# Kernel optimization log

Hardware: AMD Instinct MI355X
Metric: run time of the kernel (lower is better)

## Reference

```python
import jax, jax.numpy as jnp
import numpy as np

# Representative Blocks2Matrix configuration: single coupled block key
# (l1=2, l2=2, lambda=2), one atom type with 8 radial channels.
N_SYS = 16        # number of systems
N_ATOMS = 64      # atoms per system
L1, L2, LAM = 2, 2, 2
NRAD = 8          # radial channels per (l, Z)
S = 32768         # number of atom-pair samples across all systems
M1, M2, MU = 2 * L1 + 1, 2 * L2 + 1, 2 * LAM + 1
NORB_ATOM = NRAD * M1            # orbitals per atom (radial-major, mu-minor; see make_orbital_map)
N = N_ATOMS * NORB_ATOM          # 2560 orbitals per system


def setup_inputs() -> dict:
    key = jax.random.key(0)
    k1, k2, k3, k4, k5 = jax.random.split(key, 5)
    values = jax.random.normal(k1, (S, MU, NRAD * NRAD), dtype=jnp.float32)
    cg = jax.random.normal(k2, (M1, M2, MU), dtype=jnp.float32)
    sys_idx = jax.random.randint(k3, (S,), 0, N_SYS)
    i_idx = jax.random.randint(k4, (S,), 0, N_ATOMS)
    j_idx = jax.random.randint(k5, (S,), 0, N_ATOMS)
    return {"values": values, "cg": cg, "sys_idx": sys_idx,
            "i_idx": i_idx, "j_idx": j_idx}


def reference(values, cg, sys_idx, i_idx, j_idx):
    # Decouple: uncoupled[s, m1, m2, n1, n2] = sum_mu cg[m1, m2, mu] * values[s, mu, n1, n2]
    vals = values.reshape(S, MU, NRAD, NRAD)
    # orbital ordering is radial-major, mu-minor -> index (n, m)
    blocks = jnp.einsum('abm,smpq->spaqb', cg, vals)  # [S, n1, m1, n2, m2]
    blocks = blocks.reshape(S, NORB_ATOM, NORB_ATOM)
    # Global orbital indices for each pair's block rows/cols
    ar = jnp.arange(NORB_ATOM)
    rows = i_idx[:, None] * NORB_ATOM + ar  # [S, 40]
    cols = j_idx[:, None] * NORB_ATOM + ar  # [S, 40]
    H = jnp.zeros((N_SYS, N, N), dtype=values.dtype)
    # Scatter block at (i, j) and its transpose at (j, i) (Hermitian build)
    H = H.at[sys_idx[:, None, None], rows[:, :, None], cols[:, None, :]].add(blocks)
    H = H.at[sys_idx[:, None, None], cols[:, :, None], rows[:, None, :]].add(
        jnp.swapaxes(blocks, 1, 2))
    return H
```

## Files before the change

kernel.cpp:

```cpp
#include <hip/hip_runtime.h>


#define SS      32768
#define NORB    40
#define NSYS    16
#define NATOMS  64
#define NDIM    2560
#define NBINS   (NSYS * NATOMS * NATOMS)
#define CAP     16
#define MAXOVF  8192
#define GBLK    2048
#define TPB     256
#define WPB     (TPB / 64)
#define BPW     (NBINS / (GBLK * WPB))

#define WS_NEEDED   (524288 + (size_t)NBINS * CAP * 4)

__global__ __launch_bounds__(256) void b2m_fill(
    const int* __restrict__ sys_idx, const int* __restrict__ i_idx,
    const int* __restrict__ j_idx,
    int* __restrict__ counts, int* __restrict__ bins,
    int* __restrict__ ovf_cnt, int2* __restrict__ ovf)
{
    int s = blockIdx.x * blockDim.x + threadIdx.x;
    if (s >= SS) return;
    int sy = sys_idx[s], i = i_idx[s], j = j_idx[s];

    int bd = (sy * NATOMS + i) * NATOMS + j;
    int pos = atomicAdd(&counts[bd], 1);
    if (pos < CAP) bins[bd * CAP + pos] = s;
    else { int o = atomicAdd(ovf_cnt, 1); if (o < MAXOVF) ovf[o] = make_int2(bd, s); }

    int bt = (sy * NATOMS + j) * NATOMS + i;
    int st = s | 0x10000;
    pos = atomicAdd(&counts[bt], 1);
    if (pos < CAP) bins[bt * CAP + pos] = st;
    else { int o = atomicAdd(ovf_cnt, 1); if (o < MAXOVF) ovf[o] = make_int2(bt, st); }
}

#define ENTRY_BODY(ENT) do {                                            \
    int _ent = (ENT);                                                   \
    const float* _vb = values + (size_t)(_ent & 0xFFFF) * 320;          \
    if ((_ent & 0x10000) == 0) {                                        \
        ++nD;                                                           \
        _Pragma("unroll")                                               \
        for (int m = 0; m < 5; ++m) vsD[m] += _vb[m * 64 + lane];       \
    } else {                                                            \
        ++nT;                                                           \
        _Pragma("unroll")                                               \
        for (int m = 0; m < 5; ++m) vsT[m] += _vb[m * 64 + bsl];        \
    }                                                                   \
} while (0)

__global__ __launch_bounds__(TPB) void b2m_gather(
    const float* __restrict__ values, const float* __restrict__ cg,
    const int* __restrict__ counts, const int* __restrict__ bins,
    float* __restrict__ H)
{
    __shared__ float scg[128];
    __shared__ float stage[WPB][320];

    const int tid  = threadIdx.x;
    const int lane = tid & 63;
    const int w    = tid >> 6;

    if (tid < 125) scg[tid] = cg[tid];
    __syncthreads();

    const int p   = lane >> 3, q = lane & 7;
    const int bsl = (q << 3) | p;

    int soff[5];
    #pragma unroll
    for (int it = 0; it < 5; ++it) {
        int e = it * 64 + lane;
        int srow = e / 40, scol = e - srow * 40;
        soff[it] = srow * 5 * NDIM + scol;
    }

    const int gw = __builtin_amdgcn_readfirstlane((int)blockIdx.x * WPB + w);
    const int t0 = gw * BPW;
    float* const sw = stage[w];

    for (int t = t0; t < t0 + BPW; ++t) {
        int n = counts[t];
        if (n > CAP) n = CAP;

        float vsD[5] = {0.f, 0.f, 0.f, 0.f, 0.f};
        float vsT[5] = {0.f, 0.f, 0.f, 0.f, 0.f};
        int nD = 0, nT = 0;

        if (n > 0) {
            int4 e4 = *reinterpret_cast<const int4*>(bins + (size_t)t * CAP);
            ENTRY_BODY(e4.x);
            if (n > 1) ENTRY_BODY(e4.y);
            if (n > 2) ENTRY_BODY(e4.z);
            if (n > 3) ENTRY_BODY(e4.w);
            for (int k = 4; k < n; ++k)
                ENTRY_BODY(bins[(size_t)t * CAP + k]);
        }

        float acc[25];
        #pragma unroll
        for (int i2 = 0; i2 < 25; ++i2) acc[i2] = 0.f;

        if (nD) {
            #pragma unroll
            for (int a = 0; a < 5; ++a)
                #pragma unroll
                for (int b = 0; b < 5; ++b)
                    #pragma unroll
                    for (int m = 0; m < 5; ++m)
                        acc[a * 5 + b] = fmaf(scg[(a * 5 + b) * 5 + m], vsD[m], acc[a * 5 + b]);
        }
        if (nT) {
            #pragma unroll
            for (int a = 0; a < 5; ++a)
                #pragma unroll
                for (int b = 0; b < 5; ++b)
                    #pragma unroll
                    for (int m = 0; m < 5; ++m)
                        acc[a * 5 + b] = fmaf(scg[(b * 5 + a) * 5 + m], vsT[m], acc[a * 5 + b]);
        }

        const int jj = t & 63, ii = (t >> 6) & 63, sy = t >> 12;
        float* Hs = H + ((size_t)sy * NDIM + (size_t)ii * NORB) * NDIM + (size_t)jj * NORB;
        #pragma unroll
        for (int g = 0; g < 5; ++g) {
            #pragma unroll
            for (int b = 0; b < 5; ++b)
                sw[p * 40 + q * 5 + b] = acc[g * 5 + b];
            #pragma unroll
            for (int it = 0; it < 5; ++it)
                Hs[(size_t)(soff[it] + g * NDIM)] = sw[it * 64 + lane];
        }
    }
}

__global__ __launch_bounds__(256) void b2m_ovf_apply(
    const float* __restrict__ values, const float* __restrict__ cg,
    const int* __restrict__ ovf_cnt, const int2* __restrict__ ovf,
    float* __restrict__ H)
{
    int n = *ovf_cnt;
    if (n > MAXOVF) n = MAXOVF;
    for (int k = blockIdx.x; k < n; k += gridDim.x) {
        int  bin = ovf[k].x;
        int  ent = ovf[k].y;
        int  s   = ent & 0xFFFF;
        bool tr  = (ent >> 16) != 0;
        int  j = bin & 63, i = (bin >> 6) & 63, sy = bin >> 12;
        const float* vs = values + (size_t)s * 320;
        float* Hs = H + (size_t)sy * NDIM * NDIM;
        for (int e = threadIdx.x; e < 1600; e += blockDim.x) {
            int rr = e / 40, cc = e - rr * 40;
            int R = tr ? cc : rr, C = tr ? rr : cc;
            int pp = R / 5, a = R - pp * 5;
            int qq = C / 5, b = C - qq * 5;
            float v = 0.f;
            for (int m = 0; m < 5; ++m)
                v = fmaf(cg[(a * 5 + b) * 5 + m], vs[m * 64 + pp * 8 + qq], v);
            atomicAdd(Hs + (size_t)(i * NORB + rr) * NDIM + (j * NORB + cc), v);
        }
    }
}

__global__ __launch_bounds__(320) void b2m_scatter(
    const float* __restrict__ values, const float* __restrict__ cg,
    const int* __restrict__ sys_idx, const int* __restrict__ i_idx,
    const int* __restrict__ j_idx, float* __restrict__ H)
{
    __shared__ float svv[320];
    __shared__ float scg[125];
    const int s = blockIdx.x, tid = threadIdx.x;
    if (tid < 320) svv[tid] = values[(size_t)s * 320 + tid];
    if (tid < 125) scg[tid] = cg[tid];
    __syncthreads();
    const int sys = sys_idx[s], i = i_idx[s], j = j_idx[s];
    float* Hs = H + (size_t)sys * NDIM * NDIM;
    const int rowbase = i * NORB, colbase = j * NORB;
    #pragma unroll
    for (int it = 0; it < 5; ++it) {
        const int e = tid + it * 320;
        const int r = e / 40, c = e - r * 40;
        const int pp = r / 5, a = r - pp * 5, qq = c / 5, b = c - qq * 5;
        float v = 0.f;
        #pragma unroll
        for (int m = 0; m < 5; ++m)
            v = fmaf(scg[(a * 5 + b) * 5 + m], svv[m * 64 + pp * 8 + qq], v);
        atomicAdd(Hs + (size_t)(rowbase + r) * NDIM + (colbase + c), v);
    }
    #pragma unroll
    for (int it = 0; it < 5; ++it) {
        const int e = tid + it * 320;
        const int c2 = e / 40, r2 = e - c2 * 40;
        const int pp = r2 / 5, a = r2 - pp * 5, qq = c2 / 5, b = c2 - qq * 5;
        float v = 0.f;
        #pragma unroll
        for (int m = 0; m < 5; ++m)
            v = fmaf(scg[(a * 5 + b) * 5 + m], svv[m * 64 + pp * 8 + qq], v);
        atomicAdd(Hs + (size_t)(colbase + c2) * NDIM + (rowbase + r2), v);
    }
}

extern "C" void kernel_launch(void* const* d_in, const int* in_sizes, int n_in,
                              void* d_out, int out_size, void* d_ws, size_t ws_size,
                              hipStream_t stream) {
    const float* values  = (const float*)d_in[0];
    const float* cg      = (const float*)d_in[1];
    const int*   sys_idx = (const int*)d_in[2];
    const int*   i_idx   = (const int*)d_in[3];
    const int*   j_idx   = (const int*)d_in[4];
    float*       H       = (float*)d_out;

    if (ws_size >= WS_NEEDED) {
        char* ws      = (char*)d_ws;
        int*  counts  = (int*)ws;
        int*  ovf_cnt = (int*)(ws + 262144);
        int2* ovf     = (int2*)(ws + 262272);
        int*  bins    = (int*)(ws + 524288);

        hipMemsetAsync(ws, 0, 262400, stream);

        b2m_fill<<<(SS + 255) / 256, 256, 0, stream>>>(
            sys_idx, i_idx, j_idx, counts, bins, ovf_cnt, ovf);
        b2m_gather<<<GBLK, TPB, 0, stream>>>(values, cg, counts, bins, H);
        b2m_ovf_apply<<<64, 256, 0, stream>>>(values, cg, ovf_cnt, ovf, H);
    } else {
        hipMemsetAsync(H, 0, (size_t)out_size * sizeof(float), stream);
        b2m_scatter<<<SS, 320, 0, stream>>>(values, cg, sys_idx, i_idx, j_idx, H);
    }
}
```

Measured before the change: 617.4 us.

## Prefetch bin entries and values two tiles ahead in gather kernel

The gather kernel now loads all eight per-wave bin counts and first-entry index vectors up front, and keeps a three-slot ring buffer that issues value loads for the first entry two tiles ahead. This hides global-load latency behind the current tile's work. Empty tiles take a fast path that writes zeros directly. The CG coefficients are padded to 8 floats per row so they can be read as vector LDS loads, and the D and T contributions are fused into one FMA chain per output instead of a 25-element accumulator. The costs are higher register pressure from full unrolling and the prefetch buffers, plus an assumption that BPW equals 8.

```diff
diff --git a/kernel.cpp b/kernel.cpp
--- a/kernel.cpp
+++ b/kernel.cpp
@@ -38,33 +38,41 @@
     else { int o = atomicAdd(ovf_cnt, 1); if (o < MAXOVF) ovf[o] = make_int2(bt, st); }
 }
 
-#define ENTRY_BODY(ENT) do {                                            \
-    int _ent = (ENT);                                                   \
-    const float* _vb = values + (size_t)(_ent & 0xFFFF) * 320;          \
-    if ((_ent & 0x10000) == 0) {                                        \
-        ++nD;                                                           \
-        _Pragma("unroll")                                               \
-        for (int m = 0; m < 5; ++m) vsD[m] += _vb[m * 64 + lane];       \
-    } else {                                                            \
-        ++nT;                                                           \
-        _Pragma("unroll")                                               \
-        for (int m = 0; m < 5; ++m) vsT[m] += _vb[m * 64 + bsl];        \
-    }                                                                   \
+#define ENTRY_ADD(ENT) do {                                            \
+    const int _e = (ENT);                                              \
+    const float* _vb = values + (size_t)(_e & 0xFFFF) * 320            \
+                       + ((_e & 0x10000) ? bsl : lane);                \
+    if ((_e & 0x10000) == 0) {                                         \
+        _Pragma("unroll")                                              \
+        for (int m = 0; m < 5; ++m) vsD[m] += _vb[m * 64];             \
+    } else {                                                           \
+        _Pragma("unroll")                                              \
+        for (int m = 0; m < 5; ++m) vsT[m] += _vb[m * 64];             \
+    }                                                                  \
 } while (0)
+
+#define PV_ISSUE(SLOT, KK)                                             \
+    if ((KK) < BPW && nA[KK] > 0) {                                    \
+        const int _e0 = eb[KK].x;                                      \
+        const float* _vb = values + (size_t)(_e0 & 0xFFFF) * 320       \
+                           + ((_e0 & 0x10000) ? bsl : lane);           \
+        _Pragma("unroll")                                              \
+        for (int m = 0; m < 5; ++m) pvb[SLOT][m] = _vb[m * 64];        \
+    }
 
 __global__ __launch_bounds__(TPB) void b2m_gather(
     const float* __restrict__ values, const float* __restrict__ cg,
     const int* __restrict__ counts, const int* __restrict__ bins,
     float* __restrict__ H)
 {
-    __shared__ float scg[128];
+    __shared__ __align__(16) float scgp[25 * 8];
     __shared__ float stage[WPB][320];
 
     const int tid  = threadIdx.x;
     const int lane = tid & 63;
     const int w    = tid >> 6;
 
-    if (tid < 125) scg[tid] = cg[tid];
+    if (tid < 125) scgp[(tid / 5) * 8 + (tid % 5)] = cg[tid];
     __syncthreads();
 
     const int p   = lane >> 3, q = lane & 7;
@@ -82,54 +90,74 @@
     const int t0 = gw * BPW;
     float* const sw = stage[w];
 
-    for (int t = t0; t < t0 + BPW; ++t) {
-        int n = counts[t];
-        if (n > CAP) n = CAP;
+    int4 cA = *reinterpret_cast<const int4*>(counts + t0);
+    int4 cB = *reinterpret_cast<const int4*>(counts + t0 + 4);
+    int nA[8] = {cA.x, cA.y, cA.z, cA.w, cB.x, cB.y, cB.z, cB.w};
+    #pragma unroll
+    for (int k = 0; k < 8; ++k) if (nA[k] > CAP) nA[k] = CAP;
+
+    int4 eb[8];
+    #pragma unroll
+    for (int k = 0; k < 8; ++k)
+        eb[k] = *reinterpret_cast<const int4*>(bins + (size_t)(t0 + k) * CAP);
+
+    float pvb[3][5];
+    PV_ISSUE(0, 0)
+    PV_ISSUE(1, 1)
+
+    #pragma unroll
+    for (int k = 0; k < BPW; ++k) {
+        const int t = t0 + k;
+
+        PV_ISSUE((k + 2) % 3, k + 2)
+
+        const int jj = t & 63, ii = (t >> 6) & 63, sy = t >> 12;
+        float* Hs = H + ((size_t)sy * NDIM + (size_t)ii * NORB) * NDIM + (size_t)jj * NORB;
+
+        const int n = nA[k];
+        if (n == 0) {
+            #pragma unroll
+            for (int g = 0; g < 5; ++g)
+                #pragma unroll
+                for (int it = 0; it < 5; ++it)
+                    Hs[(size_t)(soff[it] + g * NDIM)] = 0.f;
+            continue;
+        }
 
         float vsD[5] = {0.f, 0.f, 0.f, 0.f, 0.f};
         float vsT[5] = {0.f, 0.f, 0.f, 0.f, 0.f};
-        int nD = 0, nT = 0;
-
-        if (n > 0) {
-            int4 e4 = *reinterpret_cast<const int4*>(bins + (size_t)t * CAP);
-            ENTRY_BODY(e4.x);
-            if (n > 1) ENTRY_BODY(e4.y);
-            if (n > 2) ENTRY_BODY(e4.z);
-            if (n > 3) ENTRY_BODY(e4.w);
-            for (int k = 4; k < n; ++k)
-                ENTRY_BODY(bins[(size_t)t * CAP + k]);
-        }
-
-        float acc[25];
-        #pragma unroll
-        for (int i2 = 0; i2 < 25; ++i2) acc[i2] = 0.f;
-
-        if (nD) {
-            #pragma unroll
-            for (int a = 0; a < 5; ++a)
-                #pragma unroll
-                for (int b = 0; b < 5; ++b)
-                    #pragma unroll
-                    for (int m = 0; m < 5; ++m)
-                        acc[a * 5 + b] = fmaf(scg[(a * 5 + b) * 5 + m], vsD[m], acc[a * 5 + b]);
-        }
-        if (nT) {
-            #pragma unroll
-            for (int a = 0; a < 5; ++a)
-                #pragma unroll
-                for (int b = 0; b < 5; ++b)
-                    #pragma unroll
-                    for (int m = 0; m < 5; ++m)
-                        acc[a * 5 + b] = fmaf(scg[(b * 5 + a) * 5 + m], vsT[m], acc[a * 5 + b]);
-        }
-
-        const int jj = t & 63, ii = (t >> 6) & 63, sy = t >> 12;
-        float* Hs = H + ((size_t)sy * NDIM + (size_t)ii * NORB) * NDIM + (size_t)jj * NORB;
+
+        if ((eb[k].x & 0x10000) == 0) {
+            #pragma unroll
+            for (int m = 0; m < 5; ++m) vsD[m] += pvb[k % 3][m];
+        } else {
+            #pragma unroll
+            for (int m = 0; m < 5; ++m) vsT[m] += pvb[k % 3][m];
+        }
+        if (n > 1) ENTRY_ADD(eb[k].y);
+        if (n > 2) ENTRY_ADD(eb[k].z);
+        if (n > 3) ENTRY_ADD(eb[k].w);
+        for (int kk = 4; kk < n; ++kk)
+            ENTRY_ADD(bins[(size_t)t * CAP + kk]);
+
         #pragma unroll
         for (int g = 0; g < 5; ++g) {
             #pragma unroll
-            for (int b = 0; b < 5; ++b)
-                sw[p * 40 + q * 5 + b] = acc[g * 5 + b];
+            for (int b = 0; b < 5; ++b) {
+                const float4 w0 = *reinterpret_cast<const float4*>(&scgp[(g * 5 + b) * 8]);
+                const float  w4 = scgp[(g * 5 + b) * 8 + 4];
+                const float4 u0 = *reinterpret_cast<const float4*>(&scgp[(b * 5 + g) * 8]);
+                const float  u4 = scgp[(b * 5 + g) * 8 + 4];
+                float av = fmaf(w0.x, vsD[0],
+                           fmaf(w0.y, vsD[1],
+                           fmaf(w0.z, vsD[2],
+                           fmaf(w0.w, vsD[3], w4 * vsD[4]))));
+                av = fmaf(u0.x, vsT[0],
+                     fmaf(u0.y, vsT[1],
+                     fmaf(u0.z, vsT[2],
+                     fmaf(u0.w, vsT[3], fmaf(u4, vsT[4], av)))));
+                sw[p * 40 + q * 5 + b] = av;
+            }
             #pragma unroll
             for (int it = 0; it < 5; ++it)
                 Hs[(size_t)(soff[it] + g * NDIM)] = sw[it * 64 + lane];
```

Result: faster. 557.9 us (-9.6%).
